# Optimization experiments

Hardware: AMD Instinct MI355X
Metric: run time of the kernel (lower is better)

Reference implementation:

```python
import jax, jax.numpy as jnp
import numpy as np

B, S, IN, IN2, H = 512, 256, 300, 300, 512
FN = 3  # filter_num


def setup_inputs() -> dict:
    key = jax.random.key(0)
    ks = jax.random.split(key, 16)
    def n(k, shape, scale=0.05):
        return jax.random.normal(k, shape, dtype=jnp.float32) * scale
    return {
        "x": jax.random.normal(ks[0], (B, S, IN), dtype=jnp.float32),
        "W_in": n(ks[1], (IN, IN2)), "b_in": n(ks[2], (IN2,)),
        "Wih": n(ks[3], (IN2, 4 * H)), "Whh": n(ks[4], (H, 4 * H)),
        "bih": n(ks[5], (4 * H,)), "bhh": n(ks[6], (4 * H,)),
        "Q": n(ks[7], (H, IN2)), "R": n(ks[8], (IN2, H)),
        "Wc3": n(ks[9], (FN, 1, 3, H)), "bc3": n(ks[10], (FN,)),
        "Wc4": n(ks[11], (FN, 1, 4, H)), "bc4": n(ks[12], (FN,)),
        "Wc5": n(ks[13], (FN, 1, 5, H)), "bc5": n(ks[14], (FN,)),
        "W_lin": n(ks[15], (3 * FN, 2)), "b_lin": jnp.zeros((2,), jnp.float32),
    }


def reference(x, W_in, b_in, Wih, Whh, bih, bhh, Q, R,
              Wc3, bc3, Wc4, bc4, Wc5, bc5, W_lin, b_lin):
    # input projection: [B,S,IN] -> [B,S,IN2]
    xin = jnp.tanh(x @ W_in + b_in)
    xs = jnp.swapaxes(xin, 0, 1)  # [S,B,IN2] for scan
    bsz = x.shape[0]
    h0 = jnp.zeros((bsz, H), x.dtype)
    c0 = jnp.zeros((bsz, H), x.dtype)

    def step(carry, xt):
        ht, Ct = carry
        # mogrify, mog_iterations=2: i=1 odd updates x, i=2 even updates h
        xt = 2.0 * jax.nn.sigmoid(ht @ Q) * xt
        ht = 2.0 * jax.nn.sigmoid(xt @ R) * ht
        gates = xt @ Wih + bih + ht @ Whh + bhh  # [B,4H]
        i, f, g, o = jnp.split(gates, 4, axis=1)
        Ct = jax.nn.sigmoid(f) * Ct + jax.nn.sigmoid(i) * jnp.tanh(g)
        ht = jax.nn.sigmoid(o) * jnp.tanh(Ct)
        return (ht, Ct), ht

    _, hs = jax.lax.scan(step, (h0, c0), xs)  # [S,B,H]
    hmap = jnp.swapaxes(hs, 0, 1)[:, None, :, :]  # [B,1,S,H]

    feats = []
    for w, b in ((Wc3, bc3), (Wc4, bc4), (Wc5, bc5)):
        y = jax.lax.conv_general_dilated(
            hmap, w, (1, 1), 'VALID',
            dimension_numbers=('NCHW', 'OIHW', 'NCHW'))
        y = jax.nn.relu(y + b[None, :, None, None])  # [B,FN,S-fsz+1,1]
        feats.append(jnp.max(y, axis=(2, 3)))  # global max pool -> [B,FN]
    cat = jnp.concatenate(feats, axis=1)  # [B, 3*FN]
    # dropout is identity at inference
    return cat @ W_lin + b_lin  # [B,2]
```

## Files before the change

### kernel.cpp

```cpp
#include <hip/hip_runtime.h>

#define DI __device__ __forceinline__

typedef __attribute__((ext_vector_type(4))) float  f32x4;
typedef __attribute__((ext_vector_type(8))) short  s16x8;
typedef __attribute__((ext_vector_type(8))) __bf16 bf16x8;
typedef unsigned long long u64;

constexpr int S_   = 256;
constexpr int B_   = 512;
constexpr int KP_  = 320;
constexpr int ALD_ = 832;
constexpr int NRING = 34;
constexpr int NWG  = 512;
constexpr size_t HSLOT = 512 * 512;

constexpr size_t OFF_XIN = 0;
constexpr size_t SZ_XIN  = (size_t)S_ * B_ * KP_ * 2;
constexpr size_t OFF_U   = OFF_XIN + SZ_XIN;
constexpr size_t SZ_U    = (size_t)B_ * S_ * 64 * 4;
constexpr size_t OFF_HS  = OFF_U + SZ_U;
constexpr size_t SZ_HS   = (size_t)NRING * HSLOT * 2;
constexpr size_t OFF_ACT = OFF_HS + SZ_HS;
constexpr size_t SZ_ACT  = (size_t)B_ * ALD_ * 2;
constexpr size_t OFF_WPT = OFF_ACT + SZ_ACT;
constexpr size_t SZ_WPT  = (size_t)320 * 320 * 2;
constexpr size_t OFF_QPT = OFF_WPT + SZ_WPT;
constexpr size_t SZ_QPT  = (size_t)320 * 512 * 2;
constexpr size_t OFF_RPT = OFF_QPT + SZ_QPT;
constexpr size_t SZ_RPT  = (size_t)512 * 320 * 2;
constexpr size_t OFF_WGT = OFF_RPT + SZ_RPT;
constexpr size_t SZ_WGT  = (size_t)2048 * 832 * 2;
constexpr size_t OFF_BG  = OFF_WGT + SZ_WGT;
constexpr size_t SZ_BG   = 2048 * 4;
constexpr size_t OFF_VT  = OFF_BG + SZ_BG;
constexpr size_t SZ_VT   = (size_t)64 * 512 * 2;
constexpr size_t OFF_BAR = OFF_VT + SZ_VT;
constexpr size_t SZ_BAR  = 8192;
constexpr size_t WS_NEED = OFF_BAR + SZ_BAR;

DI unsigned short f2bf(float x) {
  unsigned int u = __float_as_uint(x);
  unsigned int r = (u + 0x7FFFu + ((u >> 16) & 1u)) >> 16;
  return (unsigned short)r;
}
DI float bf2f(unsigned short h) { return __uint_as_float(((unsigned int)h) << 16); }

DI float sigm(float x) {
  float e = __builtin_amdgcn_exp2f(x * -1.44269504088896f);
  return __builtin_amdgcn_rcpf(1.0f + e);
}
DI float tanh_(float x) {
  x = fminf(fmaxf(x, -15.0f), 15.0f);
  float e = __builtin_amdgcn_exp2f(x * 2.88539008177793f);
  return (e - 1.0f) * __builtin_amdgcn_rcpf(e + 1.0f);
}
DI bf16x8 asbf(s16x8 v) { return __builtin_bit_cast(bf16x8, v); }

DI u64 ld_sys_u64(const void* p) {
  return __hip_atomic_load((const u64*)p, __ATOMIC_RELAXED, __HIP_MEMORY_SCOPE_SYSTEM);
}
DI void st_sys_u64(void* p, u64 v) {
  __hip_atomic_store((u64*)p, v, __ATOMIC_RELAXED, __HIP_MEMORY_SCOPE_SYSTEM);
}
DI unsigned int ld_sys_u32(const unsigned int* p) {
  return __hip_atomic_load(p, __ATOMIC_RELAXED, __HIP_MEMORY_SCOPE_SYSTEM);
}
DI void st_sys_u32(unsigned int* p, unsigned int v) {
  __hip_atomic_store(p, v, __ATOMIC_RELAXED, __HIP_MEMORY_SCOPE_SYSTEM);
}
template<int N> DI void wait_vm() {
  asm volatile("s_waitcnt vmcnt(%0)" :: "n"(N) : "memory");
}

template<int NK>
DI void gemm2(const unsigned short* Ab, int lda,
              const unsigned short* Bb, int ldb,
              short* sA, short* sB, f32x4 acc[2])
{
  constexpr int NR = (NK + 1) / 2;
  const int tid  = threadIdx.x;
  const int tm   = tid >> 8;
  const int t8   = tid & 255;
  const int lane = tid & 63;
  const int l15  = lane & 15;
  const int kseg = (lane >> 4) * 8;
  const int w    = (tid >> 6) & 3;
  const int wm = w >> 1, wn = w & 1;
  const int sArow = t8 >> 3, sAcol = (t8 & 7) * 4;
  const int sBrow = t8 >> 2, sBcol = (t8 & 3) * 8;
  const unsigned short* gA = Ab + sArow * lda + sAcol;
  const unsigned short* gB = Bb + sBrow * ldb + sBcol;
  short* tA = sA + tm * 2048;
  short* tB = sB + tm * 4096;
  const int aoff = sArow * 32 + sAcol;
  const int boff = sBrow * 32 + sBcol;
  const int afr  = (wm * 16 + l15) * 32 + kseg;

  u64 a0, a1 = 0, b00, b01, b10 = 0, b11 = 0;
  a0  = ld_sys_u64(gA + tm * 32);
  b00 = ((const u64*)(gB + tm * 32))[0];
  b01 = ((const u64*)(gB + tm * 32))[1];
  if (2 + tm < NK) {
    a1  = ld_sys_u64(gA + (2 + tm) * 32);
    b10 = ((const u64*)(gB + (2 + tm) * 32))[0];
    b11 = ((const u64*)(gB + (2 + tm) * 32))[1];
  }
  *(u64*)&tA[aoff] = a0;
  *(u64*)&tB[boff] = b00; *(u64*)&tB[boff + 4] = b01;
  __syncthreads();
  #pragma unroll
  for (int j = 0; j < NR; ++j) {
    const int curA = (j & 1) * 1024, curB = (j & 1) * 2048;
    if (j + 2 < NR) {
      const int kt = (j + 2) * 2 + tm;
      if (kt < NK) {
        if ((j & 1) == 0) { a0 = ld_sys_u64(gA + kt * 32);
                            b00 = ((const u64*)(gB + kt * 32))[0];
                            b01 = ((const u64*)(gB + kt * 32))[1]; }
        else              { a1 = ld_sys_u64(gA + kt * 32);
                            b10 = ((const u64*)(gB + kt * 32))[0];
                            b11 = ((const u64*)(gB + kt * 32))[1]; }
      }
    }
    if (j * 2 + tm < NK) {
      s16x8 Af = *(const s16x8*)&tA[curA + afr];
      #pragma unroll
      for (int ni = 0; ni < 2; ++ni) {
        s16x8 Bf = *(const s16x8*)&tB[curB + (wn * 32 + ni * 16 + l15) * 32 + kseg];
        acc[ni] = __builtin_amdgcn_mfma_f32_16x16x32_bf16(asbf(Af), asbf(Bf), acc[ni], 0, 0, 0);
      }
    }
    if (j + 1 < NR) {
      const int kt = (j + 1) * 2 + tm;
      const int nxtA = ((j + 1) & 1) * 1024, nxtB = ((j + 1) & 1) * 2048;
      if (kt < NK) {
        if ((j & 1) == 0) { *(u64*)&tA[nxtA + aoff] = a1;
                            *(u64*)&tB[nxtB + boff] = b10; *(u64*)&tB[nxtB + boff + 4] = b11; }
        else              { *(u64*)&tA[nxtA + aoff] = a0;
                            *(u64*)&tB[nxtB + boff] = b00; *(u64*)&tB[nxtB + boff + 4] = b01; }
      }
    }
    __syncthreads();
  }
}

DI void reduce2(f32x4 acc[2], float* rbuf) {
  const int tid = threadIdx.x, t8 = tid & 255;
  if (tid >= 256) {
    #pragma unroll
    for (int ni = 0; ni < 2; ++ni)
      #pragma unroll
      for (int r = 0; r < 4; ++r)
        rbuf[(ni * 4 + r) * 256 + t8] = acc[ni][r];
  }
  __syncthreads();
  if (tid < 256) {
    #pragma unroll
    for (int ni = 0; ni < 2; ++ni)
      #pragma unroll
      for (int r = 0; r < 4; ++r)
        acc[ni][r] += rbuf[(ni * 4 + r) * 256 + t8];
  }
}

template<typename F>
DI void epiloop32(f32x4 acc[2], F&& f) {
  const int lane = threadIdx.x & 63;
  const int w = (threadIdx.x >> 6) & 3, wm = w >> 1, wn = w & 1;
  #pragma unroll
  for (int ni = 0; ni < 2; ++ni)
    #pragma unroll
    for (int r = 0; r < 4; ++r)
      f(wm * 16 + (lane >> 4) * 4 + r, wn * 32 + ni * 16 + (lane & 15), acc[ni][r]);
}

DI void pack_store32(const unsigned short* lds16, unsigned short* dstbase, int ldd) {
  const u64* l64 = (const u64*)lds16;
  const int i = threadIdx.x;
  const int row = i >> 4, q = i & 15;
  st_sys_u64(dstbase + row * ldd + q * 4, l64[i]);
}

template<int NK, int KREAL>
DI void gemm_f32A(const float* Af, int lda,
                  const unsigned short* Bb, int ldb,
                  short* sA, short* sB, f32x4 acc[2][2])
{
  const int tid  = threadIdx.x;
  const int lane = tid & 63;
  const int w = tid >> 6, wm = w >> 1, wn = w & 1;
  const float* ga = Af + (tid >> 2) * lda;
  const int cseg  = (tid & 3) * 8;
  const unsigned short* gb = Bb + (tid >> 2) * ldb + (tid & 3) * 8;
  const int arow0 = (wm * 32 + (lane & 15)) * 32 + (lane >> 4) * 8;
  const int brow0 = (wn * 32 + (lane & 15)) * 32 + (lane >> 4) * 8;

  auto loadA = [&](int k) -> s16x8 {
    s16x8 r;
    const int c0 = k * 32 + cseg;
    if (c0 + 8 <= KREAL) {
      float4 f0 = *(const float4*)(ga + c0);
      float4 f1 = *(const float4*)(ga + c0 + 4);
      r[0] = (short)f2bf(f0.x); r[1] = (short)f2bf(f0.y);
      r[2] = (short)f2bf(f0.z); r[3] = (short)f2bf(f0.w);
      r[4] = (short)f2bf(f1.x); r[5] = (short)f2bf(f1.y);
      r[6] = (short)f2bf(f1.z); r[7] = (short)f2bf(f1.w);
    } else {
      #pragma unroll
      for (int j = 0; j < 8; ++j) {
        float x = (c0 + j < KREAL) ? ga[c0 + j] : 0.0f;
        r[j] = (short)f2bf(x);
      }
    }
    return r;
  };

  s16x8 va = loadA(0);
  s16x8 vb = *(const s16x8*)gb;
  *(s16x8*)&sA[tid * 8] = va;
  *(s16x8*)&sB[tid * 8] = vb;
  __syncthreads();
  for (int k = 0; k < NK; ++k) {
    const int cur = (k & 1) * 2048;
    if (k + 1 < NK) {
      va = loadA(k + 1);
      vb = *(const s16x8*)(gb + (k + 1) * 32);
    }
    s16x8 a0 = *(const s16x8*)&sA[cur + arow0];
    s16x8 a1 = *(const s16x8*)&sA[cur + arow0 + 16 * 32];
    s16x8 b0 = *(const s16x8*)&sB[cur + brow0];
    s16x8 b1 = *(const s16x8*)&sB[cur + brow0 + 16 * 32];
    acc[0][0] = __builtin_amdgcn_mfma_f32_16x16x32_bf16(asbf(a0), asbf(b0), acc[0][0], 0, 0, 0);
    acc[0][1] = __builtin_amdgcn_mfma_f32_16x16x32_bf16(asbf(a0), asbf(b1), acc[0][1], 0, 0, 0);
    acc[1][0] = __builtin_amdgcn_mfma_f32_16x16x32_bf16(asbf(a1), asbf(b0), acc[1][0], 0, 0, 0);
    acc[1][1] = __builtin_amdgcn_mfma_f32_16x16x32_bf16(asbf(a1), asbf(b1), acc[1][1], 0, 0, 0);
    if (k + 1 < NK) {
      const int nxt = ((k + 1) & 1) * 2048;
      *(s16x8*)&sA[nxt + tid * 8] = va;
      *(s16x8*)&sB[nxt + tid * 8] = vb;
    }
    __syncthreads();
  }
}

template<typename F>
DI void epiloop(f32x4 acc[2][2], F&& f) {
  const int lane = threadIdx.x & 63;
  const int w = (threadIdx.x & 255) >> 6, wm = w >> 1, wn = w & 1;
  #pragma unroll
  for (int mi = 0; mi < 2; ++mi)
    #pragma unroll
    for (int ni = 0; ni < 2; ++ni)
      #pragma unroll
      for (int r = 0; r < 4; ++r) {
        const int rowl = wm * 32 + mi * 16 + (lane >> 4) * 4 + r;
        const int coll = wn * 32 + ni * 16 + (lane & 15);
        f(rowl, coll, acc[mi][ni][r]);
      }
}

__global__ void k_prep_wpt(const float* __restrict__ Wi, unsigned short* __restrict__ WpT) {
  int i = blockIdx.x * 256 + threadIdx.x;
  if (i >= 320 * 320) return;
  int n = i / 320, k = i % 320;
  float v = (n < 300 && k < 300) ? Wi[k * 300 + n] : 0.0f;
  WpT[i] = f2bf(v);
}
__global__ void k_prep_qpt(const float* __restrict__ Q, unsigned short* __restrict__ QpT) {
  int i = blockIdx.x * 256 + threadIdx.x;
  if (i >= 320 * 512) return;
  int n = i >> 9, k = i & 511;
  float v = (n < 300) ? Q[k * 300 + n] : 0.0f;
  QpT[i] = f2bf(v);
}
__global__ void k_prep_rpt(const float* __restrict__ R, unsigned short* __restrict__ RpT) {
  int i = blockIdx.x * 256 + threadIdx.x;
  if (i >= 512 * 320) return;
  int n = i / 320, k = i % 320;
  float v = (k < 300) ? R[k * 512 + n] : 0.0f;
  RpT[i] = f2bf(v);
}
__global__ void k_prep_wgt(const float* __restrict__ Wih, const float* __restrict__ Whh,
                           unsigned short* __restrict__ WgT) {
  int i = blockIdx.x * 256 + threadIdx.x;
  if (i >= 2048 * 832) return;
  int np = i / 832, k = i % 832;
  int c = np >> 2, g = np & 3, col = g * 512 + c;
  float v = 0.0f;
  if (k < 300) v = Wih[k * 2048 + col];
  else if (k >= 320) v = Whh[(k - 320) * 2048 + col];
  WgT[i] = f2bf(v);
}
__global__ void k_prep_bg(const float* __restrict__ bih, const float* __restrict__ bhh,
                          float* __restrict__ bg) {
  int i = blockIdx.x * 256 + threadIdx.x;
  if (i >= 2048) return;
  int c = i >> 2, g = i & 3, col = g * 512 + c;
  bg[i] = bih[col] + bhh[col];
}
__global__ void k_prep_vt(const float* __restrict__ Wc3, const float* __restrict__ Wc4,
                          const float* __restrict__ Wc5, unsigned short* __restrict__ VT) {
  int i = blockIdx.x * 256 + threadIdx.x;
  if (i >= 64 * 512) return;
  int j = i >> 9, k = i & 511;
  float v = 0.0f;
  if (j < 9)       { int f = j / 3,  dt = j % 3;        v = Wc3[(f * 3 + dt) * 512 + k]; }
  else if (j < 21) { int jj = j - 9;  int f = jj / 4, dt = jj % 4; v = Wc4[(f * 4 + dt) * 512 + k]; }
  else if (j < 36) { int jj = j - 21; int f = jj / 5, dt = jj % 5; v = Wc5[(f * 5 + dt) * 512 + k]; }
  VT[i] = f2bf(v);
}
__global__ void k_wsfail(float* out, int n, float v) {
  int i = blockIdx.x * 256 + threadIdx.x;
  if (i < n) out[i] = -v;
}

__global__ __launch_bounds__(256) void k_proj(const float* __restrict__ x,
                                              const unsigned short* __restrict__ WpT,
                                              const float* __restrict__ b_in,
                                              unsigned short* __restrict__ xin) {
  __shared__ short sA[4096], sB[4096];
  const int m0 = blockIdx.x * 64, n0 = blockIdx.y * 64;
  f32x4 acc[2][2];
  const f32x4 z = {0.f, 0.f, 0.f, 0.f};
  acc[0][0] = z; acc[0][1] = z; acc[1][0] = z; acc[1][1] = z;
  gemm_f32A<10, 300>(x + (size_t)m0 * 300, 300, WpT + n0 * 320, 320, sA, sB, acc);
  epiloop(acc, [&](int rowl, int coll, float vacc) {
    const int row = m0 + rowl, col = n0 + coll;
    float o = 0.0f;
    if (col < 300) o = tanh_(vacc + b_in[col]);
    const int b = row >> 8, s = row & 255;
    xin[(size_t)(s * 512 + b) * KP_ + col] = f2bf(o);
  });
}

__global__ __launch_bounds__(512, 4) void k_scan(
    const unsigned short* __restrict__ xin,
    const unsigned short* __restrict__ QpT,
    const unsigned short* __restrict__ RpT,
    const unsigned short* __restrict__ WgT,
    const float* __restrict__ bg,
    const unsigned short* __restrict__ VT,
    unsigned short* __restrict__ hs,
    unsigned short* __restrict__ act,
    float* __restrict__ U,
    unsigned int* __restrict__ bar)
{
  __shared__ short sA[4096];
  __shared__ short sB[8192];
  __shared__ float rbuf[2048];
  __shared__ float gbuf[2048];
  __shared__ unsigned short pbuf[2048];
  __shared__ unsigned short obuf[2048];
  const int wg   = blockIdx.x;
  const int grp  = wg >> 5;
  const int l    = wg & 31;
  const int tid  = threadIdx.x;
  const f32x4 z = {0.f, 0.f, 0.f, 0.f};

  const int gm0 = grp * 32;
  const int gn0 = l * 64;
  float c_state = 0.f;
  const int crow = tid >> 4, ccl = tid & 15;
  const float4 cb = *(const float4*)&bg[gn0 + ccl * 4];

  unsigned int* cnt  = bar + grp * 64;
  unsigned int* p2f  = bar + grp * 64 + 32;
  int ep = 0;
  auto bar_sync = [&]() {
    wait_vm<0>();
    __syncthreads();
    if (tid == 0) {
      __hip_atomic_fetch_add(cnt, 1u, __ATOMIC_RELAXED, __HIP_MEMORY_SCOPE_AGENT);
      const unsigned tgt = (unsigned)(ep + 1) * 32u;
      while (__hip_atomic_load(cnt, __ATOMIC_RELAXED, __HIP_MEMORY_SCOPE_AGENT) < tgt)
        __builtin_amdgcn_s_sleep(1);
    }
    __syncthreads();
    ++ep;
  };

  for (int t = 0; t < S_; ++t) {
    const unsigned short* hst = hs + (size_t)(t % NRING) * HSLOT;
    unsigned short*       hso = hs + (size_t)((t + 1) % NRING) * HSLOT;

    u64 xpre = 0, hpre = 0;
    const int prow = tid >> 4, pq = tid & 15;
    if (l < 5)
      xpre = *(const u64*)(xin + ((size_t)t * 512 + gm0 + prow) * KP_ + l * 64 + pq * 4);
    if (l < 8)
      hpre = ld_sys_u64(hst + (gm0 + prow) * 512 + l * 64 + pq * 4);

    if (l < 5) {
      const int n0 = l * 64;
      ((u64*)pbuf)[tid] = xpre;
      f32x4 acc[2] = {z, z};
      gemm2<16>(hst + gm0 * 512, 512, QpT + n0 * 512, 512, sA, sB, acc);
      reduce2(acc, rbuf);
      if (tid < 256) {
        epiloop32(acc, [&](int row, int col, float v) {
          obuf[row * 64 + col] = f2bf(2.0f * sigm(v) * bf2f(pbuf[row * 64 + col]));
        });
      }
      __syncthreads();
      pack_store32(obuf, act + gm0 * ALD_ + n0, ALD_);
    }
    bar_sync();

    if (l < 8) {
      const int n0 = l * 64;
      ((u64*)pbuf)[tid] = hpre;
      f32x4 acc[2] = {z, z};
      gemm2<10>(act + gm0 * ALD_, ALD_, RpT + n0 * KP_, KP_, sA, sB, acc);
      reduce2(acc, rbuf);
      if (tid < 256) {
        epiloop32(acc, [&](int row, int col, float v) {
          obuf[row * 64 + col] = f2bf(2.0f * sigm(v) * bf2f(pbuf[row * 64 + col]));
        });
      }
      __syncthreads();
      pack_store32(obuf, act + gm0 * ALD_ + 320 + n0, ALD_);
      wait_vm<0>();
      __syncthreads();
      if (tid == 0) st_sys_u32(&p2f[l], (unsigned)(t + 1));
    }

    f32x4 acc[2] = {z, z};
    gemm2<10>(act + gm0 * ALD_, ALD_, WgT + gn0 * 832, 832, sA, sB, acc);

    {
      const unsigned tag = (unsigned)(t + 1);
      if (tid < 64) {
        while (!__all(ld_sys_u32(&p2f[tid & 7]) >= tag))
          __builtin_amdgcn_s_sleep(1);
      }
      __syncthreads();
    }

    {
      gemm2<16>(act + gm0 * ALD_ + 320, ALD_, WgT + gn0 * 832 + 320, 832, sA, sB, acc);
      reduce2(acc, rbuf);
      if (tid < 256) {
        epiloop32(acc, [&](int row, int col, float v) {
          gbuf[row * 64 + col] = v;
        });
      }
      __syncthreads();
      {
        const float iv = gbuf[crow * 64 + ccl * 4 + 0] + cb.x;
        const float fv = gbuf[crow * 64 + ccl * 4 + 1] + cb.y;
        const float gv = gbuf[crow * 64 + ccl * 4 + 2] + cb.z;
        const float ov = gbuf[crow * 64 + ccl * 4 + 3] + cb.w;
        const float cn = sigm(fv) * c_state + sigm(iv) * tanh_(gv);
        const float h  = sigm(ov) * tanh_(cn);
        c_state = cn;
        obuf[crow * 16 + ccl] = f2bf(h);
      }
      __syncthreads();
      if (tid < 128) {
        const u64* h64 = (const u64*)obuf;
        const int row = tid >> 2, q = tid & 3;
        st_sys_u64(hso + (gm0 + row) * 512 + l * 16 + q * 4, h64[row * 4 + q]);
      }
    }
    bar_sync();

    if ((t & 31) == 31) {
      const int c = t >> 5;
      const int tglob = 32 * c + l;
      const int slot = (tglob + 1) % NRING;
      f32x4 acu[2] = {z, z};
      gemm2<16>(hs + (size_t)slot * HSLOT + (size_t)gm0 * 512, 512, VT, 512, sA, sB, acu);
      reduce2(acu, rbuf);
      if (tid < 256) {
        epiloop32(acu, [&](int row, int col, float v) {
          U[((size_t)(gm0 + row) * 256 + tglob) * 64 + col] = v;
        });
      }
      __syncthreads();
    }
  }
}

__global__ __launch_bounds__(256) void k_combine(const float* __restrict__ U,
                                                 const float* __restrict__ bc3,
                                                 const float* __restrict__ bc4,
                                                 const float* __restrict__ bc5,
                                                 const float* __restrict__ Wl,
                                                 const float* __restrict__ bl,
                                                 float* __restrict__ out) {
  const int b = blockIdx.x;
  const int p = threadIdx.x;
  const float* Ub = U + (size_t)b * (256 * 64);
  float v[9];
  #pragma unroll
  for (int j = 0; j < 9; ++j) v[j] = -1e30f;
  if (p < 254) {
    #pragma unroll
    for (int f = 0; f < 3; ++f)
      v[f] = Ub[(p + 0) * 64 + f * 3 + 0] + Ub[(p + 1) * 64 + f * 3 + 1] + Ub[(p + 2) * 64 + f * 3 + 2];
  }
  if (p < 253) {
    #pragma unroll
    for (int f = 0; f < 3; ++f)
      v[3 + f] = Ub[(p + 0) * 64 + 9 + f * 4 + 0] + Ub[(p + 1) * 64 + 9 + f * 4 + 1] +
                 Ub[(p + 2) * 64 + 9 + f * 4 + 2] + Ub[(p + 3) * 64 + 9 + f * 4 + 3];
  }
  if (p < 252) {
    #pragma unroll
    for (int f = 0; f < 3; ++f)
      v[6 + f] = Ub[(p + 0) * 64 + 21 + f * 5 + 0] + Ub[(p + 1) * 64 + 21 + f * 5 + 1] +
                 Ub[(p + 2) * 64 + 21 + f * 5 + 2] + Ub[(p + 3) * 64 + 21 + f * 5 + 3] +
                 Ub[(p + 4) * 64 + 21 + f * 5 + 4];
  }
  __shared__ float red[4][9];
  const int lane = threadIdx.x & 63, w = threadIdx.x >> 6;
  #pragma unroll
  for (int j = 0; j < 9; ++j) {
    float m = v[j];
    #pragma unroll
    for (int off = 32; off >= 1; off >>= 1) m = fmaxf(m, __shfl_xor(m, off));
    if (lane == 0) red[w][j] = m;
  }
  __syncthreads();
  if (threadIdx.x < 2) {
    const int k = threadIdx.x;
    float o = bl[k];
    #pragma unroll
    for (int j = 0; j < 9; ++j) {
      float m = fmaxf(fmaxf(red[0][j], red[1][j]), fmaxf(red[2][j], red[3][j]));
      float bias = (j < 3) ? bc3[j] : (j < 6) ? bc4[j - 3] : bc5[j - 6];
      o += fmaxf(m + bias, 0.0f) * Wl[j * 2 + k];
    }
    out[b * 2 + k] = o;
  }
}

extern "C" void kernel_launch(void* const* d_in, const int* in_sizes, int n_in,
                              void* d_out, int out_size, void* d_ws, size_t ws_size,
                              hipStream_t stream) {
  const float* x     = (const float*)d_in[0];
  const float* W_in  = (const float*)d_in[1];
  const float* b_in  = (const float*)d_in[2];
  const float* Wih   = (const float*)d_in[3];
  const float* Whh   = (const float*)d_in[4];
  const float* bih   = (const float*)d_in[5];
  const float* bhh   = (const float*)d_in[6];
  const float* Q     = (const float*)d_in[7];
  const float* R     = (const float*)d_in[8];
  const float* Wc3   = (const float*)d_in[9];
  const float* bc3   = (const float*)d_in[10];
  const float* Wc4   = (const float*)d_in[11];
  const float* bc4   = (const float*)d_in[12];
  const float* Wc5   = (const float*)d_in[13];
  const float* bc5   = (const float*)d_in[14];
  const float* W_lin = (const float*)d_in[15];
  const float* b_lin = (const float*)d_in[16];

  if (ws_size < WS_NEED) {
    k_wsfail<<<4, 256, 0, stream>>>((float*)d_out, out_size, (float)(ws_size >> 20));
    return;
  }

  char* ws = (char*)d_ws;
  unsigned short* xin = (unsigned short*)(ws + OFF_XIN);
  float*          U   = (float*)(ws + OFF_U);
  unsigned short* hs  = (unsigned short*)(ws + OFF_HS);
  unsigned short* act = (unsigned short*)(ws + OFF_ACT);
  unsigned short* WpT = (unsigned short*)(ws + OFF_WPT);
  unsigned short* QpT = (unsigned short*)(ws + OFF_QPT);
  unsigned short* RpT = (unsigned short*)(ws + OFF_RPT);
  unsigned short* WgT = (unsigned short*)(ws + OFF_WGT);
  float*          bg  = (float*)(ws + OFF_BG);
  unsigned short* VT  = (unsigned short*)(ws + OFF_VT);
  unsigned int*   bar = (unsigned int*)(ws + OFF_BAR);

  (void)hipMemsetAsync(hs, 0, HSLOT * 2, stream);
  (void)hipMemsetAsync(bar, 0, SZ_BAR, stream);

  k_prep_wpt<<<(320 * 320 + 255) / 256, 256, 0, stream>>>(W_in, WpT);
  k_prep_qpt<<<(320 * 512 + 255) / 256, 256, 0, stream>>>(Q, QpT);
  k_prep_rpt<<<(512 * 320 + 255) / 256, 256, 0, stream>>>(R, RpT);
  k_prep_wgt<<<(2048 * 832 + 255) / 256, 256, 0, stream>>>(Wih, Whh, WgT);
  k_prep_bg<<<8, 256, 0, stream>>>(bih, bhh, bg);
  k_prep_vt<<<(64 * 512 + 255) / 256, 256, 0, stream>>>(Wc3, Wc4, Wc5, VT);

  k_proj<<<dim3(131072 / 64, KP_ / 64), 256, 0, stream>>>(x, WpT, b_in, xin);

  k_scan<<<NWG, 512, 0, stream>>>(xin, QpT, RpT, WgT, bg, VT, hs, act, U, bar);

  k_combine<<<512, 256, 0, stream>>>(U, bc3, bc4, bc5, W_lin, b_lin, (float*)d_out);
}
```

Baseline: 5.357 ms.

## Stage activation rows in padded LDS once and stream weights directly to MFMA

Replaces the double-buffered LDS GEMM with its split-K reduction across two 256-thread halves. The shared activation tile (32 rows, padded stride) is now loaded into LDS once per phase: h for the Q matmul, then the x/h parts of act for the R and gate matmuls. Each of the 8 waves computes one 16x16 output tile and reads B fragments straight from global memory. This removes the per-k-step barriers, the B staging and the reduction pass. In exchange, weight loads are uncoalesced per-lane global reads that are no longer shared, and bulk LDS fills are added for each phase.

```diff
diff --git a/kernel.cpp b/kernel.cpp
--- a/kernel.cpp
+++ b/kernel.cpp
@@ -11,6 +11,7 @@
 constexpr int B_   = 512;
 constexpr int KP_  = 320;
 constexpr int ALD_ = 832;
+constexpr int APAD = 844;
 constexpr int NRING = 34;
 constexpr int NWG  = 512;
 constexpr size_t HSLOT = 512 * 512;
@@ -56,6 +57,10 @@
   return (e - 1.0f) * __builtin_amdgcn_rcpf(e + 1.0f);
 }
 DI bf16x8 asbf(s16x8 v) { return __builtin_bit_cast(bf16x8, v); }
+DI s16x8 as16(u64 a, u64 b) {
+  struct P { u64 x, y; } p{a, b};
+  return __builtin_bit_cast(s16x8, p);
+}
 
 DI u64 ld_sys_u64(const void* p) {
   return __hip_atomic_load((const u64*)p, __ATOMIC_RELAXED, __HIP_MEMORY_SCOPE_SYSTEM);
@@ -74,105 +79,46 @@
 }
 
 template<int NK>
-DI void gemm2(const unsigned short* Ab, int lda,
-              const unsigned short* Bb, int ldb,
-              short* sA, short* sB, f32x4 acc[2])
+DI void gemm_stream(const short* aLds, int k0,
+                    const unsigned short* __restrict__ Bb, int ldb, f32x4& acc)
 {
-  constexpr int NR = (NK + 1) / 2;
-  const int tid  = threadIdx.x;
-  const int tm   = tid >> 8;
-  const int t8   = tid & 255;
-  const int lane = tid & 63;
-  const int l15  = lane & 15;
-  const int kseg = (lane >> 4) * 8;
-  const int w    = (tid >> 6) & 3;
-  const int wm = w >> 1, wn = w & 1;
-  const int sArow = t8 >> 3, sAcol = (t8 & 7) * 4;
-  const int sBrow = t8 >> 2, sBcol = (t8 & 3) * 8;
-  const unsigned short* gA = Ab + sArow * lda + sAcol;
-  const unsigned short* gB = Bb + sBrow * ldb + sBcol;
-  short* tA = sA + tm * 2048;
-  short* tB = sB + tm * 4096;
-  const int aoff = sArow * 32 + sAcol;
-  const int boff = sBrow * 32 + sBcol;
-  const int afr  = (wm * 16 + l15) * 32 + kseg;
-
-  u64 a0, a1 = 0, b00, b01, b10 = 0, b11 = 0;
-  a0  = ld_sys_u64(gA + tm * 32);
-  b00 = ((const u64*)(gB + tm * 32))[0];
-  b01 = ((const u64*)(gB + tm * 32))[1];
-  if (2 + tm < NK) {
-    a1  = ld_sys_u64(gA + (2 + tm) * 32);
-    b10 = ((const u64*)(gB + (2 + tm) * 32))[0];
-    b11 = ((const u64*)(gB + (2 + tm) * 32))[1];
-  }
-  *(u64*)&tA[aoff] = a0;
-  *(u64*)&tB[boff] = b00; *(u64*)&tB[boff + 4] = b01;
-  __syncthreads();
+  const int tid = threadIdx.x;
+  const int w = tid >> 6, lane = tid & 63;
+  const int l15 = lane & 15, kseg = (lane >> 4) * 8;
+  const short* ap = aLds + ((w >> 2) * 16 + l15) * APAD + k0 + kseg;
+  const unsigned short* bp = Bb + (size_t)((w & 3) * 16 + l15) * ldb + k0 + kseg;
   #pragma unroll
-  for (int j = 0; j < NR; ++j) {
-    const int curA = (j & 1) * 1024, curB = (j & 1) * 2048;
-    if (j + 2 < NR) {
-      const int kt = (j + 2) * 2 + tm;
-      if (kt < NK) {
-        if ((j & 1) == 0) { a0 = ld_sys_u64(gA + kt * 32);
-                            b00 = ((const u64*)(gB + kt * 32))[0];
-                            b01 = ((const u64*)(gB + kt * 32))[1]; }
-        else              { a1 = ld_sys_u64(gA + kt * 32);
-                            b10 = ((const u64*)(gB + kt * 32))[0];
-                            b11 = ((const u64*)(gB + kt * 32))[1]; }
-      }
-    }
-    if (j * 2 + tm < NK) {
-      s16x8 Af = *(const s16x8*)&tA[curA + afr];
-      #pragma unroll
-      for (int ni = 0; ni < 2; ++ni) {
-        s16x8 Bf = *(const s16x8*)&tB[curB + (wn * 32 + ni * 16 + l15) * 32 + kseg];
-        acc[ni] = __builtin_amdgcn_mfma_f32_16x16x32_bf16(asbf(Af), asbf(Bf), acc[ni], 0, 0, 0);
-      }
-    }
-    if (j + 1 < NR) {
-      const int kt = (j + 1) * 2 + tm;
-      const int nxtA = ((j + 1) & 1) * 1024, nxtB = ((j + 1) & 1) * 2048;
-      if (kt < NK) {
-        if ((j & 1) == 0) { *(u64*)&tA[nxtA + aoff] = a1;
-                            *(u64*)&tB[nxtB + boff] = b10; *(u64*)&tB[nxtB + boff + 4] = b11; }
-        else              { *(u64*)&tA[nxtA + aoff] = a0;
-                            *(u64*)&tB[nxtB + boff] = b00; *(u64*)&tB[nxtB + boff + 4] = b01; }
-      }
-    }
-    __syncthreads();
-  }
-}
-
-DI void reduce2(f32x4 acc[2], float* rbuf) {
-  const int tid = threadIdx.x, t8 = tid & 255;
-  if (tid >= 256) {
-    #pragma unroll
-    for (int ni = 0; ni < 2; ++ni)
-      #pragma unroll
-      for (int r = 0; r < 4; ++r)
-        rbuf[(ni * 4 + r) * 256 + t8] = acc[ni][r];
-  }
-  __syncthreads();
-  if (tid < 256) {
-    #pragma unroll
-    for (int ni = 0; ni < 2; ++ni)
-      #pragma unroll
-      for (int r = 0; r < 4; ++r)
-        acc[ni][r] += rbuf[(ni * 4 + r) * 256 + t8];
+  for (int kt = 0; kt < NK; ++kt) {
+    s16x8 a = *(const s16x8*)(ap + kt * 32);
+    s16x8 b = *(const s16x8*)(bp + kt * 32);
+    acc = __builtin_amdgcn_mfma_f32_16x16x32_bf16(asbf(a), asbf(b), acc, 0, 0, 0);
+  }
+}
+
+DI void gemm_gA16(const unsigned short* __restrict__ Ag, int lda,
+                  const unsigned short* __restrict__ Bb, int ldb, f32x4& acc)
+{
+  const int tid = threadIdx.x;
+  const int w = tid >> 6, lane = tid & 63;
+  const int l15 = lane & 15, kseg = (lane >> 4) * 8;
+  const unsigned short* ap = Ag + (size_t)((w >> 2) * 16 + l15) * lda + kseg;
+  const unsigned short* bp = Bb + (size_t)((w & 3) * 16 + l15) * ldb + kseg;
+  #pragma unroll
+  for (int kt = 0; kt < 16; ++kt) {
+    s16x8 a = as16(ld_sys_u64(ap + kt * 32), ld_sys_u64(ap + kt * 32 + 4));
+    s16x8 b = *(const s16x8*)(bp + kt * 32);
+    acc = __builtin_amdgcn_mfma_f32_16x16x32_bf16(asbf(a), asbf(b), acc, 0, 0, 0);
   }
 }
 
 template<typename F>
-DI void epiloop32(f32x4 acc[2], F&& f) {
-  const int lane = threadIdx.x & 63;
-  const int w = (threadIdx.x >> 6) & 3, wm = w >> 1, wn = w & 1;
+DI void epi16(f32x4 acc, F&& f) {
+  const int tid = threadIdx.x;
+  const int w = tid >> 6, lane = tid & 63;
+  const int r0 = (w >> 2) * 16 + (lane >> 4) * 4;
+  const int c  = (w & 3) * 16 + (lane & 15);
   #pragma unroll
-  for (int ni = 0; ni < 2; ++ni)
-    #pragma unroll
-    for (int r = 0; r < 4; ++r)
-      f(wm * 16 + (lane >> 4) * 4 + r, wn * 32 + ni * 16 + (lane & 15), acc[ni][r]);
+  for (int r = 0; r < 4; ++r) f(r0 + r, c, acc[r]);
 }
 
 DI void pack_store32(const unsigned short* lds16, unsigned short* dstbase, int ldd) {
@@ -346,9 +292,7 @@
     float* __restrict__ U,
     unsigned int* __restrict__ bar)
 {
-  __shared__ short sA[4096];
-  __shared__ short sB[8192];
-  __shared__ float rbuf[2048];
+  __shared__ __align__(16) short aLds[32 * APAD];
   __shared__ float gbuf[2048];
   __shared__ unsigned short pbuf[2048];
   __shared__ unsigned short obuf[2048];
@@ -364,8 +308,8 @@
   const int crow = tid >> 4, ccl = tid & 15;
   const float4 cb = *(const float4*)&bg[gn0 + ccl * 4];
 
-  unsigned int* cnt  = bar + grp * 64;
-  unsigned int* p2f  = bar + grp * 64 + 32;
+  unsigned int* cnt = bar + grp * 64;
+  unsigned int* p2f = bar + grp * 64 + 32;
   int ep = 0;
   auto bar_sync = [&]() {
     wait_vm<0>();
@@ -380,9 +324,12 @@
     ++ep;
   };
 
+  for (int i = tid; i < 32 * APAD; i += 512) aLds[i] = 0;
+  __syncthreads();
+
   for (int t = 0; t < S_; ++t) {
+    unsigned short* hso = hs + (size_t)((t + 1) % NRING) * HSLOT;
     const unsigned short* hst = hs + (size_t)(t % NRING) * HSLOT;
-    unsigned short*       hso = hs + (size_t)((t + 1) % NRING) * HSLOT;
 
     u64 xpre = 0, hpre = 0;
     const int prow = tid >> 4, pq = tid & 15;
@@ -392,41 +339,46 @@
       hpre = ld_sys_u64(hst + (gm0 + prow) * 512 + l * 64 + pq * 4);
 
     if (l < 5) {
-      const int n0 = l * 64;
       ((u64*)pbuf)[tid] = xpre;
-      f32x4 acc[2] = {z, z};
-      gemm2<16>(hst + gm0 * 512, 512, QpT + n0 * 512, 512, sA, sB, acc);
-      reduce2(acc, rbuf);
-      if (tid < 256) {
-        epiloop32(acc, [&](int row, int col, float v) {
-          obuf[row * 64 + col] = f2bf(2.0f * sigm(v) * bf2f(pbuf[row * 64 + col]));
-        });
-      }
-      __syncthreads();
-      pack_store32(obuf, act + gm0 * ALD_ + n0, ALD_);
+      f32x4 acc = z;
+      gemm_stream<16>(aLds, 0, QpT + (size_t)(l * 64) * 512, 512, acc);
+      __syncthreads();
+      epi16(acc, [&](int row, int col, float v) {
+        obuf[row * 64 + col] = f2bf(2.0f * sigm(v) * bf2f(pbuf[row * 64 + col]));
+      });
+      __syncthreads();
+      pack_store32(obuf, act + gm0 * ALD_ + l * 64, ALD_);
     }
     bar_sync();
 
+    {
+      #pragma unroll
+      for (int it = 0; it < 5; ++it) {
+        const int i = it * 512 + tid;
+        const int row = i / 80, q = i - row * 80;
+        *(u64*)&aLds[row * APAD + q * 4] =
+          ld_sys_u64(act + (gm0 + row) * ALD_ + q * 4);
+      }
+      __syncthreads();
+    }
+
     if (l < 8) {
-      const int n0 = l * 64;
       ((u64*)pbuf)[tid] = hpre;
-      f32x4 acc[2] = {z, z};
-      gemm2<10>(act + gm0 * ALD_, ALD_, RpT + n0 * KP_, KP_, sA, sB, acc);
-      reduce2(acc, rbuf);
-      if (tid < 256) {
-        epiloop32(acc, [&](int row, int col, float v) {
-          obuf[row * 64 + col] = f2bf(2.0f * sigm(v) * bf2f(pbuf[row * 64 + col]));
-        });
-      }
-      __syncthreads();
-      pack_store32(obuf, act + gm0 * ALD_ + 320 + n0, ALD_);
+      f32x4 acc = z;
+      gemm_stream<10>(aLds, 0, RpT + (size_t)(l * 64) * KP_, KP_, acc);
+      __syncthreads();
+      epi16(acc, [&](int row, int col, float v) {
+        obuf[row * 64 + col] = f2bf(2.0f * sigm(v) * bf2f(pbuf[row * 64 + col]));
+      });
+      __syncthreads();
+      pack_store32(obuf, act + gm0 * ALD_ + 320 + l * 64, ALD_);
       wait_vm<0>();
       __syncthreads();
       if (tid == 0) st_sys_u32(&p2f[l], (unsigned)(t + 1));
     }
 
-    f32x4 acc[2] = {z, z};
-    gemm2<10>(act + gm0 * ALD_, ALD_, WgT + gn0 * 832, 832, sA, sB, acc);
+    f32x4 acc = z;
+    gemm_stream<10>(aLds, 0, WgT + (size_t)gn0 * 832, 832, acc);
 
     {
       const unsigned tag = (unsigned)(t + 1);
@@ -438,13 +390,21 @@
     }
 
     {
-      gemm2<16>(act + gm0 * ALD_ + 320, ALD_, WgT + gn0 * 832 + 320, 832, sA, sB, acc);
-      reduce2(acc, rbuf);
-      if (tid < 256) {
-        epiloop32(acc, [&](int row, int col, float v) {
-          gbuf[row * 64 + col] = v;
-        });
-      }
+      #pragma unroll
+      for (int it = 0; it < 8; ++it) {
+        const int i = it * 512 + tid;
+        const int row = i >> 7, q = i & 127;
+        *(u64*)&aLds[row * APAD + 320 + q * 4] =
+          ld_sys_u64(act + (gm0 + row) * ALD_ + 320 + q * 4);
+      }
+      __syncthreads();
+    }
+
+    {
+      gemm_stream<16>(aLds, 320, WgT + (size_t)gn0 * 832, 832, acc);
+      epi16(acc, [&](int row, int col, float v) {
+        gbuf[row * 64 + col] = v;
+      });
       __syncthreads();
       {
         const float iv = gbuf[crow * 64 + ccl * 4 + 0] + cb.x;
@@ -465,19 +425,26 @@
     }
     bar_sync();
 
+    {
+      #pragma unroll
+      for (int it = 0; it < 8; ++it) {
+        const int i = it * 512 + tid;
+        const int row = i >> 7, q = i & 127;
+        *(u64*)&aLds[row * APAD + q * 4] =
+          ld_sys_u64(hso + (gm0 + row) * 512 + q * 4);
+      }
+      __syncthreads();
+    }
+
     if ((t & 31) == 31) {
       const int c = t >> 5;
       const int tglob = 32 * c + l;
       const int slot = (tglob + 1) % NRING;
-      f32x4 acu[2] = {z, z};
-      gemm2<16>(hs + (size_t)slot * HSLOT + (size_t)gm0 * 512, 512, VT, 512, sA, sB, acu);
-      reduce2(acu, rbuf);
-      if (tid < 256) {
-        epiloop32(acu, [&](int row, int col, float v) {
-          U[((size_t)(gm0 + row) * 256 + tglob) * 64 + col] = v;
-        });
-      }
-      __syncthreads();
+      f32x4 acu = z;
+      gemm_gA16(hs + (size_t)slot * HSLOT + (size_t)gm0 * 512, 512, VT, 512, acu);
+      epi16(acu, [&](int row, int col, float v) {
+        U[((size_t)(gm0 + row) * 256 + tglob) * 64 + col] = v;
+      });
     }
   }
 }
```

New measurement: 8.895 ms. 1.66x slower.
